# Performance work log

Hardware: AMD Instinct MI355X
Metric: run time of the kernel (lower is better)

Reference implementation:

```python
import jax, jax.numpy as jnp
import numpy as np

B, S, D = 2, 2048, 1024
E, N, HID = 8, 4, 4096

def setup_inputs() -> dict:
    key = jax.random.key(0)
    ks = jax.random.split(key, 6)
    x = jax.random.normal(ks[0], (B, S, D), dtype=jnp.float32)
    w_router = jax.random.normal(ks[1], (E, D), dtype=jnp.float32) * 0.02
    A_fc = jax.random.normal(ks[2], (E, N, N, N), dtype=jnp.float32) * 0.5
    S_fc = jax.random.normal(ks[3], (E, N, HID // N, D // N), dtype=jnp.float32) * (1.0 / np.sqrt(D))
    A_proj = jax.random.normal(ks[4], (E, N, N, N), dtype=jnp.float32) * 0.5
    S_proj = jax.random.normal(ks[5], (E, N, D // N, HID // N), dtype=jnp.float32) * (1.0 / np.sqrt(HID))
    return {"x": x, "w_router": w_router, "A_fc": A_fc, "S_fc": S_fc, "A_proj": A_proj, "S_proj": S_proj}

def _phm(Xn, A, S):
    # Xn: [T, n, s_in], S: [n, s_out, s_in], A: [n, n, n] -> [T, n, s_out]
    T_ = jnp.einsum('bkl,iol->bkio', Xn, S)
    return jnp.einsum('ijk,bkio->bjo', A, T_)

def reference(x, w_router, A_fc, S_fc, A_proj, S_proj):
    e_num, n = A_fc.shape[0], A_fc.shape[1]
    d = x.shape[-1]
    flat = x.reshape(-1, d)                      # [T, D]
    T = flat.shape[0]
    logits = flat @ w_router.T                   # [T, E]
    probs = jax.nn.softmax(logits, axis=-1)
    expert_idx = jnp.argmax(logits, axis=-1)     # [T]
    tpe = jnp.zeros((e_num,), flat.dtype).at[expert_idx].add(1.0)
    frac = tpe / T
    aux_loss = jnp.sum(frac * probs.mean(axis=0)) * e_num
    Xn = flat.reshape(T, n, d // n)
    out = jnp.zeros_like(flat)
    for e in range(e_num):                        # small fixed expert loop
        h = _phm(Xn, A_fc[e], S_fc[e]).reshape(T, -1)   # [T, HID]
        h = jnp.where(h >= 0, h, 0.5 * h)               # leaky_relu slope 0.5
        Hn = (h * h).reshape(T, n, -1)
        y = _phm(Hn, A_proj[e], S_proj[e]).reshape(T, d)
        out = out + jnp.where((expert_idx == e)[:, None], y, jnp.zeros((), flat.dtype))
    return out.reshape(x.shape), aux_loss
```

## Files before the change

### kernel.cpp

```cpp
#include <hip/hip_runtime.h>
#include <hip/hip_bf16.h>


#define T_TOK 4096
#define DIM   1024
#define NEXP  8
#define HIDD  4096
#define SLOTS 5120

static constexpr size_t OFF_WFC   = 0;
static constexpr size_t OFF_WPROJ = 67108864ull;
static constexpr size_t OFF_XG    = 134217728ull;
static constexpr size_t OFF_H     = 144703488ull;
static constexpr size_t OFF_PROBS = 186646528ull;
static constexpr size_t OFF_EIDX  = OFF_PROBS + (size_t)T_TOK*8*4;
static constexpr size_t OFF_TOK   = OFF_EIDX + (size_t)T_TOK*4;
static constexpr size_t OFF_CNT   = OFF_TOK + (size_t)SLOTS*4;
static constexpr size_t OFF_SLOT  = OFF_CNT + 1024;

typedef __attribute__((ext_vector_type(8))) short short8;
typedef __attribute__((ext_vector_type(4))) float f32x4;

static __device__ __forceinline__ ushort f2bf(float f) {
    __hip_bfloat16 h = __float2bfloat16(f);
    return __builtin_bit_cast(ushort, h);
}

static __device__ __forceinline__ void gload_lds16(const ushort* g, ushort* l) {
    __builtin_amdgcn_global_load_lds((const __attribute__((address_space(1))) void*)g,
                                     (__attribute__((address_space(3))) void*)l,
                                     16, 0, 0);
}

__global__ __launch_bounds__(256) void router_k(const float* __restrict__ x,
                                                const float* __restrict__ wr,
                                                float* __restrict__ probs,
                                                int* __restrict__ eidx)
{
    int tid = threadIdx.x, w = tid >> 6, lane = tid & 63;
    int t = blockIdx.x * 4 + w;
    const float4* xr = (const float4*)(x + (size_t)t * DIM);
    float4 xv[4];
#pragma unroll
    for (int q = 0; q < 4; q++) xv[q] = xr[q * 64 + lane];
    double lg[8];
#pragma unroll
    for (int e = 0; e < 8; e++) {
        const float4* wv = (const float4*)(wr + (size_t)e * DIM);
        double s = 0.0;
#pragma unroll
        for (int q = 0; q < 4; q++) {
            float4 a = xv[q], b = wv[q * 64 + lane];
            s += (double)a.x * b.x + (double)a.y * b.y + (double)a.z * b.z + (double)a.w * b.w;
        }
#pragma unroll
        for (int d = 1; d < 64; d <<= 1) s += __shfl_xor(s, d);
        lg[e] = s;
    }
    double m = lg[0];
#pragma unroll
    for (int e = 1; e < 8; e++) m = lg[e] > m ? lg[e] : m;
    double ex[8], sum = 0.0;
#pragma unroll
    for (int e = 0; e < 8; e++) { ex[e] = exp(lg[e] - m); sum += ex[e]; }
    if (lane < 8) probs[(size_t)t * 8 + lane] = (float)(ex[lane] / sum);
    if (lane == 0) {
        int am = 0; double bv = lg[0];
#pragma unroll
        for (int e = 1; e < 8; e++) if (lg[e] > bv) { bv = lg[e]; am = e; }
        eidx[t] = am;
    }
}

__global__ __launch_bounds__(256) void plan_k(const float* __restrict__ probs,
                                              const int* __restrict__ eidx,
                                              int* __restrict__ counts,
                                              int* __restrict__ offsets,
                                              int* __restrict__ slot,
                                              int* __restrict__ tok,
                                              float* __restrict__ auxout)
{
    __shared__ int hist[256][8];
    __shared__ double red[256][8];
    __shared__ int offs[8];
    int tid = threadIdx.x;
    for (int i = tid; i < SLOTS; i += 256) tok[i] = -1;
    int base = tid * 16;
    int le[16];
    int lc[8] = {0,0,0,0,0,0,0,0};
#pragma unroll
    for (int j = 0; j < 16; j++) { le[j] = eidx[base + j]; lc[le[j]]++; }
#pragma unroll
    for (int e = 0; e < 8; e++) hist[tid][e] = lc[e];
    __syncthreads();
    for (int s = 1; s < 256; s <<= 1) {
        int v[8];
        if (tid >= s) {
#pragma unroll
            for (int e = 0; e < 8; e++) v[e] = hist[tid - s][e];
        }
        __syncthreads();
        if (tid >= s) {
#pragma unroll
            for (int e = 0; e < 8; e++) hist[tid][e] += v[e];
        }
        __syncthreads();
    }
    int myBase[8];
#pragma unroll
    for (int e = 0; e < 8; e++) myBase[e] = hist[tid][e] - lc[e];
    if (tid == 0) {
        int off = 0;
#pragma unroll
        for (int e = 0; e < 8; e++) {
            int c = hist[255][e];
            counts[e] = c;
            offsets[e] = off; offs[e] = off;
            off += (c + 127) & ~127;
        }
    }
    __syncthreads();
    int cur[8];
#pragma unroll
    for (int e = 0; e < 8; e++) cur[e] = myBase[e];
#pragma unroll
    for (int j = 0; j < 16; j++) {
        int e = le[j];
        int s_ = offs[e] + cur[e]++;
        slot[base + j] = s_;
        tok[s_] = base + j;
    }
    double ps[8] = {0, 0, 0, 0, 0, 0, 0, 0};
    for (int t = tid; t < T_TOK; t += 256) {
#pragma unroll
        for (int e = 0; e < 8; e++) ps[e] += (double)probs[(size_t)t * 8 + e];
    }
#pragma unroll
    for (int e = 0; e < 8; e++) red[tid][e] = ps[e];
    __syncthreads();
    for (int s = 128; s > 0; s >>= 1) {
        if (tid < s) {
#pragma unroll
            for (int e = 0; e < 8; e++) red[tid][e] += red[tid + s][e];
        }
        __syncthreads();
    }
    if (tid == 0) {
        double aux = 0.0;
#pragma unroll
        for (int e = 0; e < 8; e++)
            aux += ((double)hist[255][e] / T_TOK) * (red[0][e] / T_TOK);
        auxout[0] = (float)(aux * NEXP);
    }
}

__global__ __launch_bounds__(256) void gather_k(const float* __restrict__ x,
                                                const int* __restrict__ slot,
                                                ushort* __restrict__ xg)
{
    int tid = threadIdx.x, w = tid >> 6, lane = tid & 63;
    int t = blockIdx.x * 4 + w;
    int s = slot[t];
    const float4* xr = (const float4*)(x + (size_t)t * DIM);
    ushort4* xo = (ushort4*)(xg + (size_t)s * DIM);
#pragma unroll
    for (int q = 0; q < 4; q++) {
        float4 v = xr[q * 64 + lane];
        ushort4 b;
        b.x = f2bf(v.x); b.y = f2bf(v.y); b.z = f2bf(v.z); b.w = f2bf(v.w);
        xo[q * 64 + lane] = b;
    }
}

__global__ __launch_bounds__(256) void wfc_k(const float* __restrict__ A,
                                             const float* __restrict__ S,
                                             ushort* __restrict__ W)
{
    int b = blockIdx.x;
    int e = b >> 10, o = b & 1023;
    int l = threadIdx.x;
    __shared__ float Ash[64];
    if (l < 64) Ash[l] = A[e * 64 + l];
    __syncthreads();
    float s0 = S[((size_t)(e * 4 + 0) * 1024 + o) * 256 + l];
    float s1 = S[((size_t)(e * 4 + 1) * 1024 + o) * 256 + l];
    float s2 = S[((size_t)(e * 4 + 2) * 1024 + o) * 256 + l];
    float s3 = S[((size_t)(e * 4 + 3) * 1024 + o) * 256 + l];
    size_t base = (size_t)e * 4194304ull;
#pragma unroll
    for (int j = 0; j < 4; j++)
#pragma unroll
        for (int k = 0; k < 4; k++) {
            float v = Ash[j * 4 + k] * s0 + Ash[16 + j * 4 + k] * s1 +
                      Ash[32 + j * 4 + k] * s2 + Ash[48 + j * 4 + k] * s3;
            W[base + (size_t)(j * 1024 + o) * 1024 + k * 256 + l] = f2bf(v);
        }
}

__global__ __launch_bounds__(256) void wpj_k(const float* __restrict__ A,
                                             const float* __restrict__ S,
                                             ushort* __restrict__ W)
{
    int b = blockIdx.x;
    int e = b >> 8, o = b & 255;
    int tid = threadIdx.x;
    __shared__ float Ash[64];
    if (tid < 64) Ash[tid] = A[e * 64 + tid];
    __syncthreads();
    float s[4][4];
#pragma unroll
    for (int i = 0; i < 4; i++)
#pragma unroll
        for (int q = 0; q < 4; q++)
            s[i][q] = S[((size_t)(e * 4 + i) * 256 + o) * 1024 + q * 256 + tid];
    size_t base = (size_t)e * 4194304ull;
#pragma unroll
    for (int j = 0; j < 4; j++)
#pragma unroll
        for (int k = 0; k < 4; k++) {
            float a0 = Ash[j * 4 + k], a1 = Ash[16 + j * 4 + k];
            float a2 = Ash[32 + j * 4 + k], a3 = Ash[48 + j * 4 + k];
#pragma unroll
            for (int q = 0; q < 4; q++) {
                float v = a0 * s[0][q] + a1 * s[1][q] + a2 * s[2][q] + a3 * s[3][q];
                W[base + (size_t)(j * 256 + o) * 4096 + k * 1024 + q * 256 + tid] = f2bf(v);
            }
        }
}

template <int KDIM, int NDIM, int NSPLIT, bool FC>
__global__ __launch_bounds__(256, 4) void moe_gemm_k(const ushort* __restrict__ Abuf,
                                                     const ushort* __restrict__ Wbuf,
                                                     ushort* __restrict__ Hout,
                                                     float* __restrict__ Yout,
                                                     const int* __restrict__ counts,
                                                     const int* __restrict__ offsets)
{
    __shared__ __align__(16) ushort As[128 * 64];
    __shared__ __align__(16) ushort Bs[128 * 64];
    constexpr int NBY = NDIM / 128;
    constexpr int YPX = NBY / 8;
    constexpr int KSUB = KDIM / NSPLIT;
    constexpr int NT = KSUB / 64;
    int b = blockIdx.x;
    int r = b >> 3;
    int nb = (b & 7) * YPX + r / (40 * NSPLIT);
    int rem = r % (40 * NSPLIT);
    int split = rem / 40;
    int ms = rem % 40;
    int e = -1, mt = 0, acct = 0;
#pragma unroll
    for (int i = 0; i < 8; i++) {
        int tiles = (counts[i] + 127) >> 7;
        if (e < 0 && ms < acct + tiles) { e = i; mt = ms - acct; }
        acct += tiles;
    }
    if (e < 0) return;
    int m_base = offsets[e] + mt * 128;
    int n_base = nb * 128;
    int tid = threadIdx.x, w = tid >> 6, lane = tid & 63;
    int wm = w >> 1, wn = w & 1;
    const ushort* Ab = Abuf + (size_t)m_base * KDIM + split * KSUB;
    const ushort* Bb = Wbuf + (size_t)e * NDIM * KDIM + (size_t)n_base * KDIM + split * KSUB;
    int lr = lane >> 3;
    int lcs = (((lane & 7) ^ lr) << 3);
    f32x4 acc[4][4];
#pragma unroll
    for (int i = 0; i < 4; i++)
#pragma unroll
        for (int j = 0; j < 4; j++) acc[i][j] = (f32x4){0.f, 0.f, 0.f, 0.f};

    for (int t = 0; t < NT; t++) {
        int k0 = t * 64;
#pragma unroll
        for (int i = 0; i < 4; i++) {
            int r0 = i * 32 + w * 8;
            gload_lds16(Ab + (size_t)(r0 + lr) * KDIM + k0 + lcs, As + r0 * 64);
            gload_lds16(Bb + (size_t)(r0 + lr) * KDIM + k0 + lcs, Bs + r0 * 64);
        }
        __syncthreads();
#pragma unroll
        for (int ks = 0; ks < 2; ks++) {
            short8 a[4], bfr[4];
#pragma unroll
            for (int f = 0; f < 4; f++) {
                int ra = wm * 64 + f * 16 + (lane & 15);
                int ca = (((ks * 4 + (lane >> 4)) ^ (lane & 7)) << 3);
                a[f] = *(const short8*)&As[ra * 64 + ca];
                int rb = wn * 64 + f * 16 + (lane & 15);
                bfr[f] = *(const short8*)&Bs[rb * 64 + ca];
            }
#pragma unroll
            for (int mf = 0; mf < 4; mf++)
#pragma unroll
                for (int nf = 0; nf < 4; nf++)
                    acc[mf][nf] = __builtin_amdgcn_mfma_f32_16x16x32_bf16(a[mf], bfr[nf], acc[mf][nf], 0, 0, 0);
        }
        __syncthreads();
    }

    int col0 = n_base + wn * 64;
    int row0 = wm * 64 + (lane >> 4) * 4;
    if (FC) {
#pragma unroll
        for (int mf = 0; mf < 4; mf++)
#pragma unroll
            for (int nf = 0; nf < 4; nf++) {
                int col = col0 + nf * 16 + (lane & 15);
#pragma unroll
                for (int rg = 0; rg < 4; rg++) {
                    float v = acc[mf][nf][rg];
                    v = v >= 0.f ? v : 0.5f * v;
                    v = v * v;
                    Hout[(size_t)(m_base + row0 + mf * 16 + rg) * NDIM + col] = f2bf(v);
                }
            }
    } else {
        float* P = Yout + (size_t)split * SLOTS * NDIM;
#pragma unroll
        for (int mf = 0; mf < 4; mf++)
#pragma unroll
            for (int nf = 0; nf < 4; nf++) {
                int col = col0 + nf * 16 + (lane & 15);
#pragma unroll
                for (int rg = 0; rg < 4; rg++)
                    P[(size_t)(m_base + row0 + mf * 16 + rg) * NDIM + col] = acc[mf][nf][rg];
            }
    }
}

__global__ __launch_bounds__(256) void reduce_k(const float* __restrict__ P,
                                                const int* __restrict__ tok,
                                                float* __restrict__ out)
{
    int slot = blockIdx.x;
    int t = tok[slot];
    if (t < 0) return;
    const float4* p0 = (const float4*)(P + (size_t)slot * DIM);
    const float4* p1 = (const float4*)(P + (size_t)(SLOTS + slot) * DIM);
    float4* o = (float4*)(out + (size_t)t * DIM);
    int i = threadIdx.x;
    float4 a = p0[i], b = p1[i];
    o[i] = (float4){a.x + b.x, a.y + b.y, a.z + b.z, a.w + b.w};
}

extern "C" void kernel_launch(void* const* d_in, const int* in_sizes, int n_in,
                              void* d_out, int out_size, void* d_ws, size_t ws_size,
                              hipStream_t stream)
{
    const float* x    = (const float*)d_in[0];
    const float* wr   = (const float*)d_in[1];
    const float* A_fc = (const float*)d_in[2];
    const float* S_fc = (const float*)d_in[3];
    const float* A_pj = (const float*)d_in[4];
    const float* S_pj = (const float*)d_in[5];
    float* out = (float*)d_out;
    char* ws = (char*)d_ws;

    ushort* Wfc   = (ushort*)(ws + OFF_WFC);
    float*  Part  = (float*)(ws + OFF_WFC);
    ushort* Wpj   = (ushort*)(ws + OFF_WPROJ);
    ushort* xg    = (ushort*)(ws + OFF_XG);
    ushort* h     = (ushort*)(ws + OFF_H);
    float*  probs = (float*)(ws + OFF_PROBS);
    int*    eidx  = (int*)(ws + OFF_EIDX);
    int*    tok   = (int*)(ws + OFF_TOK);
    int*    counts  = (int*)(ws + OFF_CNT);
    int*    offsets = counts + 16;
    int*    slot  = (int*)(ws + OFF_SLOT);

    router_k<<<T_TOK / 4, 256, 0, stream>>>(x, wr, probs, eidx);
    plan_k<<<1, 256, 0, stream>>>(probs, eidx, counts, offsets, slot, tok,
                                  out + (size_t)T_TOK * DIM);
    gather_k<<<T_TOK / 4, 256, 0, stream>>>(x, slot, xg);
    wfc_k<<<NEXP * 1024, 256, 0, stream>>>(A_fc, S_fc, Wfc);
    wpj_k<<<NEXP * 256, 256, 0, stream>>>(A_pj, S_pj, Wpj);
    moe_gemm_k<1024, 4096, 1, true><<<1280, 256, 0, stream>>>(xg, Wfc, h, nullptr, counts, offsets);
    moe_gemm_k<4096, 1024, 2, false><<<640, 256, 0, stream>>>(h, Wpj, nullptr, Part, counts, offsets);
    reduce_k<<<SLOTS, 256, 0, stream>>>(Part, tok, out);
}
```

Baseline: 204.8 us.

## Fuse bf16 cast into router, gather rows in GEMM, widen N tile to 256

The separate gather kernel is removed. The router now writes a bf16 copy of x in token order, and the FC GEMM gathers rows through the tok index while loading A into LDS. Both expert GEMMs use a 128x256 tile with 4x8 MFMA fragments per wave, which halves the grid and raises reuse of each A tile. The cost is a larger accumulator and LDS footprint (occupancy hint lowered to 2 blocks per SIMD) and fewer blocks to fill the CUs.

```diff
diff --git a/kernel.cpp b/kernel.cpp
--- a/kernel.cpp
+++ b/kernel.cpp
@@ -10,13 +10,12 @@
 
 static constexpr size_t OFF_WFC   = 0;
 static constexpr size_t OFF_WPROJ = 67108864ull;
-static constexpr size_t OFF_XG    = 134217728ull;
+static constexpr size_t OFF_XB    = 134217728ull;
 static constexpr size_t OFF_H     = 144703488ull;
 static constexpr size_t OFF_PROBS = 186646528ull;
 static constexpr size_t OFF_EIDX  = OFF_PROBS + (size_t)T_TOK*8*4;
 static constexpr size_t OFF_TOK   = OFF_EIDX + (size_t)T_TOK*4;
 static constexpr size_t OFF_CNT   = OFF_TOK + (size_t)SLOTS*4;
-static constexpr size_t OFF_SLOT  = OFF_CNT + 1024;
 
 typedef __attribute__((ext_vector_type(8))) short short8;
 typedef __attribute__((ext_vector_type(4))) float f32x4;
@@ -35,7 +34,8 @@
 __global__ __launch_bounds__(256) void router_k(const float* __restrict__ x,
                                                 const float* __restrict__ wr,
                                                 float* __restrict__ probs,
-                                                int* __restrict__ eidx)
+                                                int* __restrict__ eidx,
+                                                ushort* __restrict__ xb)
 {
     int tid = threadIdx.x, w = tid >> 6, lane = tid & 63;
     int t = blockIdx.x * 4 + w;
@@ -43,6 +43,14 @@
     float4 xv[4];
 #pragma unroll
     for (int q = 0; q < 4; q++) xv[q] = xr[q * 64 + lane];
+    ushort4* xo = (ushort4*)(xb + (size_t)t * DIM);
+#pragma unroll
+    for (int q = 0; q < 4; q++) {
+        float4 v = xv[q];
+        ushort4 bq;
+        bq.x = f2bf(v.x); bq.y = f2bf(v.y); bq.z = f2bf(v.z); bq.w = f2bf(v.w);
+        xo[q * 64 + lane] = bq;
+    }
     double lg[8];
 #pragma unroll
     for (int e = 0; e < 8; e++) {
@@ -76,7 +84,6 @@
                                               const int* __restrict__ eidx,
                                               int* __restrict__ counts,
                                               int* __restrict__ offsets,
-                                              int* __restrict__ slot,
                                               int* __restrict__ tok,
                                               float* __restrict__ auxout)
 {
@@ -126,9 +133,7 @@
 #pragma unroll
     for (int j = 0; j < 16; j++) {
         int e = le[j];
-        int s_ = offs[e] + cur[e]++;
-        slot[base + j] = s_;
-        tok[s_] = base + j;
+        tok[offs[e] + cur[e]++] = base + j;
     }
     double ps[8] = {0, 0, 0, 0, 0, 0, 0, 0};
     for (int t = tid; t < T_TOK; t += 256) {
@@ -151,24 +156,6 @@
         for (int e = 0; e < 8; e++)
             aux += ((double)hist[255][e] / T_TOK) * (red[0][e] / T_TOK);
         auxout[0] = (float)(aux * NEXP);
-    }
-}
-
-__global__ __launch_bounds__(256) void gather_k(const float* __restrict__ x,
-                                                const int* __restrict__ slot,
-                                                ushort* __restrict__ xg)
-{
-    int tid = threadIdx.x, w = tid >> 6, lane = tid & 63;
-    int t = blockIdx.x * 4 + w;
-    int s = slot[t];
-    const float4* xr = (const float4*)(x + (size_t)t * DIM);
-    ushort4* xo = (ushort4*)(xg + (size_t)s * DIM);
-#pragma unroll
-    for (int q = 0; q < 4; q++) {
-        float4 v = xr[q * 64 + lane];
-        ushort4 b;
-        b.x = f2bf(v.x); b.y = f2bf(v.y); b.z = f2bf(v.z); b.w = f2bf(v.w);
-        xo[q * 64 + lane] = b;
     }
 }
 
@@ -229,25 +216,30 @@
 }
 
 template <int KDIM, int NDIM, int NSPLIT, bool FC>
-__global__ __launch_bounds__(256, 4) void moe_gemm_k(const ushort* __restrict__ Abuf,
+__global__ __launch_bounds__(256, 2) void moe_gemm_k(const ushort* __restrict__ Abuf,
                                                      const ushort* __restrict__ Wbuf,
                                                      ushort* __restrict__ Hout,
                                                      float* __restrict__ Yout,
                                                      const int* __restrict__ counts,
-                                                     const int* __restrict__ offsets)
+                                                     const int* __restrict__ offsets,
+                                                     const int* __restrict__ tok)
 {
     __shared__ __align__(16) ushort As[128 * 64];
-    __shared__ __align__(16) ushort Bs[128 * 64];
-    constexpr int NBY = NDIM / 128;
-    constexpr int YPX = NBY / 8;
+    __shared__ __align__(16) ushort Bs[256 * 64];
     constexpr int KSUB = KDIM / NSPLIT;
     constexpr int NT = KSUB / 64;
     int b = blockIdx.x;
-    int r = b >> 3;
-    int nb = (b & 7) * YPX + r / (40 * NSPLIT);
-    int rem = r % (40 * NSPLIT);
-    int split = rem / 40;
-    int ms = rem % 40;
+    int nb, split, ms;
+    if (FC) {
+        int r = b >> 3;
+        nb = (b & 7) * 2 + r / 40;
+        split = 0;
+        ms = r % 40;
+    } else {
+        nb = (b & 7) >> 1;
+        split = b & 1;
+        ms = b >> 3;
+    }
     int e = -1, mt = 0, acct = 0;
 #pragma unroll
     for (int i = 0; i < 8; i++) {
@@ -257,55 +249,68 @@
     }
     if (e < 0) return;
     int m_base = offsets[e] + mt * 128;
-    int n_base = nb * 128;
+    int n_base = nb * 256;
     int tid = threadIdx.x, w = tid >> 6, lane = tid & 63;
     int wm = w >> 1, wn = w & 1;
-    const ushort* Ab = Abuf + (size_t)m_base * KDIM + split * KSUB;
-    const ushort* Bb = Wbuf + (size_t)e * NDIM * KDIM + (size_t)n_base * KDIM + split * KSUB;
+    const ushort* Bb = Wbuf + (size_t)e * NDIM * KDIM + (size_t)n_base * KDIM;
     int lr = lane >> 3;
     int lcs = (((lane & 7) ^ lr) << 3);
-    f32x4 acc[4][4];
+    const ushort* arow[4];
+#pragma unroll
+    for (int i = 0; i < 4; i++) {
+        int sl = m_base + i * 32 + w * 8 + lr;
+        int rt = sl;
+        if (FC) { rt = tok[sl]; if (rt < 0) rt = 0; }
+        arow[i] = Abuf + (size_t)rt * KDIM + lcs;
+    }
+    f32x4 acc[4][8];
 #pragma unroll
     for (int i = 0; i < 4; i++)
 #pragma unroll
-        for (int j = 0; j < 4; j++) acc[i][j] = (f32x4){0.f, 0.f, 0.f, 0.f};
+        for (int j = 0; j < 8; j++) acc[i][j] = (f32x4){0.f, 0.f, 0.f, 0.f};
 
     for (int t = 0; t < NT; t++) {
-        int k0 = t * 64;
-#pragma unroll
-        for (int i = 0; i < 4; i++) {
+        int k0 = split * KSUB + t * 64;
+#pragma unroll
+        for (int i = 0; i < 4; i++)
+            gload_lds16(arow[i] + k0, &As[(i * 32 + w * 8) * 64]);
+#pragma unroll
+        for (int i = 0; i < 8; i++) {
             int r0 = i * 32 + w * 8;
-            gload_lds16(Ab + (size_t)(r0 + lr) * KDIM + k0 + lcs, As + r0 * 64);
-            gload_lds16(Bb + (size_t)(r0 + lr) * KDIM + k0 + lcs, Bs + r0 * 64);
+            gload_lds16(Bb + (size_t)(r0 + lr) * KDIM + k0 + lcs, &Bs[r0 * 64]);
         }
         __syncthreads();
 #pragma unroll
         for (int ks = 0; ks < 2; ks++) {
-            short8 a[4], bfr[4];
+            short8 a[4], bfr[8];
 #pragma unroll
             for (int f = 0; f < 4; f++) {
                 int ra = wm * 64 + f * 16 + (lane & 15);
                 int ca = (((ks * 4 + (lane >> 4)) ^ (lane & 7)) << 3);
                 a[f] = *(const short8*)&As[ra * 64 + ca];
-                int rb = wn * 64 + f * 16 + (lane & 15);
+            }
+#pragma unroll
+            for (int f = 0; f < 8; f++) {
+                int rb = wn * 128 + f * 16 + (lane & 15);
+                int ca = (((ks * 4 + (lane >> 4)) ^ (lane & 7)) << 3);
                 bfr[f] = *(const short8*)&Bs[rb * 64 + ca];
             }
 #pragma unroll
             for (int mf = 0; mf < 4; mf++)
 #pragma unroll
-                for (int nf = 0; nf < 4; nf++)
+                for (int nf = 0; nf < 8; nf++)
                     acc[mf][nf] = __builtin_amdgcn_mfma_f32_16x16x32_bf16(a[mf], bfr[nf], acc[mf][nf], 0, 0, 0);
         }
         __syncthreads();
     }
 
-    int col0 = n_base + wn * 64;
+    int col0 = n_base + wn * 128;
     int row0 = wm * 64 + (lane >> 4) * 4;
     if (FC) {
 #pragma unroll
         for (int mf = 0; mf < 4; mf++)
 #pragma unroll
-            for (int nf = 0; nf < 4; nf++) {
+            for (int nf = 0; nf < 8; nf++) {
                 int col = col0 + nf * 16 + (lane & 15);
 #pragma unroll
                 for (int rg = 0; rg < 4; rg++) {
@@ -320,7 +325,7 @@
 #pragma unroll
         for (int mf = 0; mf < 4; mf++)
 #pragma unroll
-            for (int nf = 0; nf < 4; nf++) {
+            for (int nf = 0; nf < 8; nf++) {
                 int col = col0 + nf * 16 + (lane & 15);
 #pragma unroll
                 for (int rg = 0; rg < 4; rg++)
@@ -360,22 +365,20 @@
     ushort* Wfc   = (ushort*)(ws + OFF_WFC);
     float*  Part  = (float*)(ws + OFF_WFC);
     ushort* Wpj   = (ushort*)(ws + OFF_WPROJ);
-    ushort* xg    = (ushort*)(ws + OFF_XG);
+    ushort* xb    = (ushort*)(ws + OFF_XB);
     ushort* h     = (ushort*)(ws + OFF_H);
     float*  probs = (float*)(ws + OFF_PROBS);
     int*    eidx  = (int*)(ws + OFF_EIDX);
     int*    tok   = (int*)(ws + OFF_TOK);
     int*    counts  = (int*)(ws + OFF_CNT);
     int*    offsets = counts + 16;
-    int*    slot  = (int*)(ws + OFF_SLOT);
-
-    router_k<<<T_TOK / 4, 256, 0, stream>>>(x, wr, probs, eidx);
-    plan_k<<<1, 256, 0, stream>>>(probs, eidx, counts, offsets, slot, tok,
+
+    router_k<<<T_TOK / 4, 256, 0, stream>>>(x, wr, probs, eidx, xb);
+    plan_k<<<1, 256, 0, stream>>>(probs, eidx, counts, offsets, tok,
                                   out + (size_t)T_TOK * DIM);
-    gather_k<<<T_TOK / 4, 256, 0, stream>>>(x, slot, xg);
     wfc_k<<<NEXP * 1024, 256, 0, stream>>>(A_fc, S_fc, Wfc);
     wpj_k<<<NEXP * 256, 256, 0, stream>>>(A_pj, S_pj, Wpj);
-    moe_gemm_k<1024, 4096, 1, true><<<1280, 256, 0, stream>>>(xg, Wfc, h, nullptr, counts, offsets);
-    moe_gemm_k<4096, 1024, 2, false><<<640, 256, 0, stream>>>(h, Wpj, nullptr, Part, counts, offsets);
+    moe_gemm_k<1024, 4096, 1, true><<<640, 256, 0, stream>>>(xb, Wfc, h, nullptr, counts, offsets, tok);
+    moe_gemm_k<4096, 1024, 2, false><<<320, 256, 0, stream>>>(h, Wpj, nullptr, Part, counts, offsets, tok);
     reduce_k<<<SLOTS, 256, 0, stream>>>(Part, tok, out);
 }
```

Result: faster. 190.9 us (-6.8%).
